# Kernel optimization log

Measured on AMD Instinct MI355X. Metric: run time of the kernel, lower is better.

Reference implementation:

```python
import jax, jax.numpy as jnp
import numpy as np

N_NODES, T, C_IN, B = 207, 12, 4, 4
NT = N_NODES * T
D, H = 96, 4
HD = D // H
FF = 4 * D
ENC_L, DEC_L = 4, 1
N_MASK = int(NT * 0.75)
N_UNMASK = NT - N_MASK
MAX_NEIGH = 40
ATTN_SCALE = 1.0 / float(np.sqrt(HD))
SQRT_D = float(np.sqrt(D))


def _ln(x, g, b, eps=1e-5):
    m = jnp.mean(x, -1, keepdims=True)
    v = jnp.mean((x - m) ** 2, -1, keepdims=True)
    return (x - m) * jax.lax.rsqrt(v + eps) * g + b


def _transformer(x, attn_mask, layers):
    # x: [B, S, D]; attn_mask: [S, S] bool (True = disallowed) or None.
    x = x * SQRT_D  # nn.Transformer-style input scaling
    def step(h, p):
        aw, ab, W1, B1, W2, B2, LN = p
        Bq, S, _ = h.shape
        q = (h @ aw[0] + ab[0]).reshape(Bq, S, H, HD)
        k = (h @ aw[1] + ab[1]).reshape(Bq, S, H, HD)
        v = (h @ aw[2] + ab[2]).reshape(Bq, S, H, HD)
        scores = jnp.einsum('bqhd,bkhd->bhqk', q, k) * ATTN_SCALE
        if attn_mask is not None:
            scores = jnp.where(attn_mask, jnp.float32(-1e30), scores)
        probs = jax.nn.softmax(scores, axis=-1)
        o = jnp.einsum('bhqk,bkhd->bqhd', probs, v).reshape(Bq, S, D)
        h = _ln(h + o @ aw[3] + ab[3], LN[0, 0], LN[0, 1])  # post-norm (torch default)
        f = jax.nn.relu(h @ W1 + B1) @ W2 + B2
        h = _ln(h + f, LN[1, 0], LN[1, 1])
        return h, None
    x, _ = jax.lax.scan(step, x, layers)
    return x


def _layer_params(key, nlayers):
    ks = jax.random.split(key, 3)
    attn_w = jax.random.normal(ks[0], (nlayers, 4, D, D), jnp.float32) / float(np.sqrt(D))
    w1 = jax.random.normal(ks[1], (nlayers, D, FF), jnp.float32) / float(np.sqrt(D))
    w2 = jax.random.normal(ks[2], (nlayers, FF, D), jnp.float32) / float(np.sqrt(FF))
    ln = jnp.broadcast_to(jnp.stack([jnp.ones(D), jnp.zeros(D)]), (nlayers, 2, 2, D)).astype(jnp.float32)
    return (attn_w, jnp.zeros((nlayers, 4, D), jnp.float32), w1,
            jnp.zeros((nlayers, FF), jnp.float32), w2, jnp.zeros((nlayers, D), jnp.float32), ln)


def setup_inputs() -> dict:
    key = jax.random.key(0)
    ks = jax.random.split(key, 12)
    rng = np.random.default_rng(42)
    perm = rng.permutation(NT)
    masked_idx = jnp.asarray(np.sort(perm[:N_MASK]), jnp.int32)
    unmasked_idx = jnp.asarray(np.sort(perm[N_MASK:]), jnp.int32)
    ea = _layer_params(ks[3], ENC_L)
    da = _layer_params(ks[4], DEC_L)
    return dict(
        history_data=jax.random.uniform(ks[0], (B, T, N_NODES, C_IN), jnp.float32),
        unmasked_idx=unmasked_idx, masked_idx=masked_idx,
        nodevec1=jax.random.normal(ks[1], (N_NODES, 10), jnp.float32),
        nodevec2=jax.random.normal(ks[2], (10, N_NODES), jnp.float32),
        dim_w=jax.random.normal(ks[5], (1, D), jnp.float32),
        dim_b=jnp.zeros((D,), jnp.float32),
        pos_emb=jax.random.uniform(ks[6], (NT, D), jnp.float32, -0.02, 0.02),
        tod_w=jax.random.normal(ks[7], (1, D), jnp.float32) * 0.02,
        tod_b=jnp.zeros((D,), jnp.float32),
        dow_w=jax.random.normal(ks[8], (1, D), jnp.float32) * 0.02,
        dow_b=jnp.zeros((D,), jnp.float32),
        mask_token=jax.random.normal(ks[9], (D,), jnp.float32) * 0.02,
        enc_attn_w=ea[0], enc_attn_b=ea[1], enc_ffn_w1=ea[2], enc_ffn_b1=ea[3],
        enc_ffn_w2=ea[4], enc_ffn_b2=ea[5], enc_ln=ea[6],
        enc_norm_g=jnp.ones((D,), jnp.float32), enc_norm_b=jnp.zeros((D,), jnp.float32),
        e2d_w=jax.random.normal(ks[10], (D, D), jnp.float32) / float(np.sqrt(D)),
        e2d_b=jnp.zeros((D,), jnp.float32),
        dec_attn_w=da[0], dec_attn_b=da[1], dec_ffn_w1=da[2], dec_ffn_b1=da[3],
        dec_ffn_w2=da[4], dec_ffn_b2=da[5], dec_ln=da[6],
        dec_norm_g=jnp.ones((D,), jnp.float32), dec_norm_b=jnp.zeros((D,), jnp.float32),
        out_w=jax.random.normal(ks[11], (D, 1), jnp.float32) / float(np.sqrt(D)),
        out_b=jnp.zeros((1,), jnp.float32),
    )


def reference(history_data, unmasked_idx, masked_idx, nodevec1, nodevec2,
              dim_w, dim_b, pos_emb, tod_w, tod_b, dow_w, dow_b, mask_token,
              enc_attn_w, enc_attn_b, enc_ffn_w1, enc_ffn_b1, enc_ffn_w2, enc_ffn_b2, enc_ln,
              enc_norm_g, enc_norm_b, e2d_w, e2d_b,
              dec_attn_w, dec_attn_b, dec_ffn_w1, dec_ffn_b1, dec_ffn_w2, dec_ffn_b2, dec_ln,
              dec_norm_g, dec_norm_b, out_w, out_b):
    hist = jnp.transpose(history_data, (0, 2, 3, 1))  # [B, N, C, T]
    tod = hist[:, :, 3:4, :].reshape(B, NT, 1)
    dow = hist[:, :, 2:3, :].reshape(B, NT, 1)
    # --- adaptive graph: softmax(relu(v1 v2)), threshold + top-40, straight-through ---
    A = jax.nn.softmax(jax.nn.relu(nodevec1 @ nodevec2), axis=1)
    kth = -jnp.sort(-A, axis=1)[:, MAX_NEIGH:MAX_NEIGH + 1]  # (MAX_NEIGH+1)-th largest per row
    keep = jnp.logical_and(A > 1.0 / N_NODES, A > kth).astype(A.dtype)
    bin_mask = jax.lax.stop_gradient(keep - A) + A
    adpA = A * bin_mask
    adpA_full = jnp.repeat(jnp.repeat(adpA, T, axis=0), T, axis=1)  # [NT, NT] block structure
    # --- embed + positional/temporal encoding ---
    x = jnp.transpose(hist[:, :, 0:1, :], (0, 1, 3, 2)) @ dim_w + dim_b  # [B, N, T, D]
    token = x.reshape(B, NT, D) + pos_emb + (tod @ tod_w + tod_b) + (dow @ dow_w + dow_b)
    # --- encoder over unmasked tokens with graph-derived attention mask ---
    enc_in = token[:, unmasked_idx, :]
    A_sub = adpA_full[unmasked_idx][:, unmasked_idx]
    attn_mask = A_sub == 0  # ~A.bool(): True = disallowed
    h = _transformer(enc_in, attn_mask,
                     (enc_attn_w, enc_attn_b, enc_ffn_w1, enc_ffn_b1, enc_ffn_w2, enc_ffn_b2, enc_ln))
    h = _ln(h, enc_norm_g, enc_norm_b)
    # --- decoder ---
    h = h @ e2d_w + e2d_b
    h_masked = (mask_token[None, None, :] + pos_emb[masked_idx]
                + (tod[:, masked_idx] @ tod_w + tod_b)
                + (dow[:, masked_idx] @ dow_w + dow_b))  # [B, N_MASK, D]
    full = jnp.concatenate([h, h_masked], axis=1)  # [B, NT, D]
    full = _transformer(full, None,
                        (dec_attn_w, dec_attn_b, dec_ffn_w1, dec_ffn_b1, dec_ffn_w2, dec_ffn_b2, dec_ln))
    full = _ln(full, dec_norm_g, dec_norm_b)
    recon = full @ out_w + out_b  # [B, NT, 1]
    recon_masked = recon[:, N_UNMASK:, :]
    label = jnp.transpose(hist, (0, 1, 3, 2))[:, :, :, 0].reshape(B, NT, 1)
    label_masked = label[:, masked_idx, :]
    return recon_masked, label_masked
```

## Files before the change

### kernel.cpp

```cpp
#include <hip/hip_runtime.h>
#include <math.h>

#define N_NODES 207
#define T_STEPS 12
#define NT 2484
#define BQ 4
#define DIM 96
#define NH 4
#define HD 24
#define FFD 384
#define N_MASK 1863
#define N_UNMASK 621
#define MAX_NEIGH 40
#define ATTN_SCALE 0.20412414523193154f
#define SQRT_DF 9.797958971132712f
#define KT 256
#define NMW 20
#define NBH 16

static inline int cdiv(int a, int b) { return (a + b - 1) / b; }

__global__ __launch_bounds__(256) void adj_kernel(const float* __restrict__ nv1,
                                                  const float* __restrict__ nv2,
                                                  float* __restrict__ keep) {
    int r = blockIdx.x, t = threadIdx.x;
    __shared__ float a[N_NODES];
    __shared__ float red[256];
    __shared__ int   redi[256];
    __shared__ int   taken[N_NODES];
    __shared__ float v1[10];
    __shared__ float kth;
    if (t < 10) v1[t] = nv1[r * 10 + t];
    __syncthreads();
    if (t < N_NODES) {
        float s = 0.f;
#pragma unroll
        for (int c = 0; c < 10; ++c) s += v1[c] * nv2[c * N_NODES + t];
        a[t] = fmaxf(s, 0.f);
        taken[t] = 0;
    }
    __syncthreads();
    red[t] = (t < N_NODES) ? a[t] : -3e38f;
    __syncthreads();
    for (int s = 128; s > 0; s >>= 1) {
        if (t < s) red[t] = fmaxf(red[t], red[t + s]);
        __syncthreads();
    }
    float mx = red[0];
    __syncthreads();
    float e = 0.f;
    if (t < N_NODES) e = __expf(a[t] - mx);
    red[t] = e;
    __syncthreads();
    for (int s = 128; s > 0; s >>= 1) {
        if (t < s) red[t] += red[t + s];
        __syncthreads();
    }
    float inv = 1.f / red[0];
    __syncthreads();
    if (t < N_NODES) a[t] = e * inv;
    __syncthreads();
    for (int round = 0; round <= MAX_NEIGH; ++round) {
        red[t]  = (t < N_NODES && !taken[t]) ? a[t] : -1.f;
        redi[t] = t;
        __syncthreads();
        for (int s = 128; s > 0; s >>= 1) {
            if (t < s && red[t + s] > red[t]) { red[t] = red[t + s]; redi[t] = redi[t + s]; }
            __syncthreads();
        }
        if (t == 0) {
            taken[redi[0]] = 1;
            if (round == MAX_NEIGH) kth = red[0];
        }
        __syncthreads();
    }
    if (t < N_NODES) {
        float av = a[t];
        keep[r * N_NODES + t] = (av > (1.f / 207.f) && av > kth) ? 1.f : 0.f;
    }
}

__global__ void maskbits_kernel(const float* __restrict__ keep, const int* __restrict__ uidx,
                                unsigned int* __restrict__ mw) {
    int q = blockIdx.x;
    int w = threadIdx.x;
    if (w >= NMW) return;
    const float* krow = keep + (uidx[q] / T_STEPS) * N_NODES;
    unsigned int word = 0;
    for (int j = 0; j < 32; ++j) {
        int k = w * 32 + j;
        if (k < N_UNMASK && krow[uidx[k] / T_STEPS] != 0.f) word |= (1u << j);
    }
    mw[q * NMW + w] = word;
}

__global__ void encin_kernel(const float* __restrict__ hist, const int* __restrict__ uidx,
                             const float* __restrict__ dim_w, const float* __restrict__ dim_b,
                             const float* __restrict__ pos,
                             const float* __restrict__ tod_w, const float* __restrict__ tod_b,
                             const float* __restrict__ dow_w, const float* __restrict__ dow_b,
                             float* __restrict__ h) {
    int idx = blockIdx.x * blockDim.x + threadIdx.x;
    if (idx >= BQ * N_UNMASK * DIM) return;
    int d = idx % DIM;
    int q = (idx / DIM) % N_UNMASK;
    int b = idx / (DIM * N_UNMASK);
    int u = uidx[q];
    int n = u / T_STEPS, t = u % T_STEPS;
    const float* hp = hist + ((size_t)(b * T_STEPS + t) * N_NODES + n) * 4;
    float h0 = hp[0], dw = hp[2], td = hp[3];
    float val = h0 * dim_w[d] + dim_b[d] + pos[u * DIM + d]
              + td * tod_w[d] + tod_b[d] + dw * dow_w[d] + dow_b[d];
    h[idx] = val * SQRT_DF;
}

__global__ void hmasked_kernel(const float* __restrict__ hist, const int* __restrict__ midx,
                               const float* __restrict__ mask_token, const float* __restrict__ pos,
                               const float* __restrict__ tod_w, const float* __restrict__ tod_b,
                               const float* __restrict__ dow_w, const float* __restrict__ dow_b,
                               float* __restrict__ full) {
    int idx = blockIdx.x * blockDim.x + threadIdx.x;
    if (idx >= BQ * N_MASK * DIM) return;
    int d = idx % DIM;
    int j = (idx / DIM) % N_MASK;
    int b = idx / (DIM * N_MASK);
    int m = midx[j];
    int n = m / T_STEPS, t = m % T_STEPS;
    const float* hp = hist + ((size_t)(b * T_STEPS + t) * N_NODES + n) * 4;
    float dw = hp[2], td = hp[3];
    float val = mask_token[d] + pos[m * DIM + d]
              + td * tod_w[d] + tod_b[d] + dw * dow_w[d] + dow_b[d];
    full[((size_t)(b * NT) + N_UNMASK + j) * DIM + d] = val * SQRT_DF;
}

__global__ void label_kernel(const float* __restrict__ hist, const int* __restrict__ midx,
                             float* __restrict__ out) {
    int idx = blockIdx.x * blockDim.x + threadIdx.x;
    if (idx >= BQ * N_MASK) return;
    int j = idx % N_MASK;
    int b = idx / N_MASK;
    int m = midx[j];
    int n = m / T_STEPS, t = m % T_STEPS;
    out[BQ * N_MASK + idx] = hist[((size_t)(b * T_STEPS + t) * N_NODES + n) * 4 + 0];
}

#define ACCROW(accv, av)                                          \
    accv.x += av.x*w0.x + av.y*w1.x + av.z*w2.x + av.w*w3.x;      \
    accv.y += av.x*w0.y + av.y*w1.y + av.z*w2.y + av.w*w3.y;      \
    accv.z += av.x*w0.z + av.y*w1.z + av.z*w2.z + av.w*w3.z;      \
    accv.w += av.x*w0.w + av.y*w1.w + av.z*w2.w + av.w*w3.w;

template<int WMODE, int LNA>
__global__ __launch_bounds__(256) void tgemm_kernel(const float* __restrict__ A,
                                                    const float* __restrict__ W,
                                                    const float* __restrict__ bias,
                                                    const float* __restrict__ res,
                                                    float* __restrict__ C,
                                                    int M, int N, int K, int gm,
                                                    int relu, float scale, int rmode,
                                                    const float* __restrict__ g1,
                                                    const float* __restrict__ b1,
                                                    const float* __restrict__ g2,
                                                    const float* __restrict__ b2,
                                                    float* __restrict__ wb) {
    __shared__ float As[64][100];
    __shared__ float Ws[96][64];
    __shared__ float lred[64][4];
    __shared__ float lmv[64][2];
    int tid = threadIdx.x;
    int bm = blockIdx.x % gm;
    int bn = blockIdx.x / gm;
    int m0 = bm * 64, n0 = bn * 64;
    int tn4 = (tid & 15) * 4;
    int tm4 = (tid >> 4) * 4;
    float4 acc0 = {0,0,0,0}, acc1 = {0,0,0,0}, acc2 = {0,0,0,0}, acc3 = {0,0,0,0};

    for (int kc = 0; kc < K; kc += 96) {
        if (kc) __syncthreads();
#pragma unroll
        for (int i = 0; i < 6; ++i) {
            int f = i * 256 + tid;
            int r = f / 24, c4 = (f % 24) * 4;
            float4 v = {0,0,0,0};
            if (m0 + r < M) v = *(const float4*)(A + (size_t)(m0 + r) * K + kc + c4);
            *(float4*)&As[r][c4] = v;
        }
#pragma unroll
        for (int i = 0; i < 6; ++i) {
            int f = i * 256 + tid;
            int kr = f >> 4, n4 = (f & 15) * 4;
            int gn = n0 + n4;
            float4 v = {0,0,0,0};
            if (gn < N) {
                if (WMODE == 0) {
                    v = *(const float4*)(W + (size_t)(kc + kr) * N + gn);
                } else {
                    int gg = gn / 96, nc = gn - gg * 96;
                    v = *(const float4*)(W + (size_t)gg * 9216 + (kc + kr) * 96 + nc);
                }
            }
            *(float4*)&Ws[kr][n4] = v;
        }
        __syncthreads();

        if (LNA > 0 && kc == 0) {
#pragma unroll
            for (int pass = 0; pass < LNA; ++pass) {
                const float* lg = pass ? g2 : g1;
                const float* lb = pass ? b2 : b1;
                int row = tid >> 2, part = tid & 3;
                float s = 0.f;
                for (int c = part * 24; c < part * 24 + 24; ++c) s += As[row][c];
                lred[row][part] = s;
                __syncthreads();
                float mean = (lred[row][0] + lred[row][1] + lred[row][2] + lred[row][3]) * (1.f / 96.f);
                float s2 = 0.f;
                for (int c = part * 24; c < part * 24 + 24; ++c) {
                    float d = As[row][c] - mean; s2 += d * d;
                }
                __syncthreads();
                lred[row][part] = s2;
                __syncthreads();
                if (part == 0) {
                    float var = (lred[row][0] + lred[row][1] + lred[row][2] + lred[row][3]) * (1.f / 96.f);
                    lmv[row][0] = mean;
                    lmv[row][1] = rsqrtf(var + 1e-5f);
                }
                __syncthreads();
#pragma unroll
                for (int i = 0; i < 6; ++i) {
                    int f = i * 256 + tid;
                    int r = f / 24, c4 = (f % 24) * 4;
                    float mn = lmv[r][0], rsd = lmv[r][1];
                    float4 v = *(float4*)&As[r][c4];
                    v.x = (v.x - mn) * rsd * lg[c4 + 0] + lb[c4 + 0];
                    v.y = (v.y - mn) * rsd * lg[c4 + 1] + lb[c4 + 1];
                    v.z = (v.z - mn) * rsd * lg[c4 + 2] + lb[c4 + 2];
                    v.w = (v.w - mn) * rsd * lg[c4 + 3] + lb[c4 + 3];
                    *(float4*)&As[r][c4] = v;
                }
                __syncthreads();
            }
            if (wb && bn == 0) {
#pragma unroll
                for (int i = 0; i < 6; ++i) {
                    int f = i * 256 + tid;
                    int r = f / 24, c4 = (f % 24) * 4;
                    if (m0 + r < M)
                        *(float4*)(wb + (size_t)(m0 + r) * 96 + c4) = *(const float4*)&As[r][c4];
                }
            }
        }

#pragma unroll 4
        for (int k = 0; k < 96; k += 4) {
            float4 a0 = *(const float4*)&As[tm4 + 0][k];
            float4 a1 = *(const float4*)&As[tm4 + 1][k];
            float4 a2 = *(const float4*)&As[tm4 + 2][k];
            float4 a3 = *(const float4*)&As[tm4 + 3][k];
            float4 w0 = *(const float4*)&Ws[k + 0][tn4];
            float4 w1 = *(const float4*)&Ws[k + 1][tn4];
            float4 w2 = *(const float4*)&Ws[k + 2][tn4];
            float4 w3 = *(const float4*)&Ws[k + 3][tn4];
            ACCROW(acc0, a0)
            ACCROW(acc1, a1)
            ACCROW(acc2, a2)
            ACCROW(acc3, a3)
        }
    }

    int gn = n0 + tn4;
    if (gn >= N) return;
    float4 bv = *(const float4*)(bias + gn);
    float4 av[4] = {acc0, acc1, acc2, acc3};
#pragma unroll
    for (int i = 0; i < 4; ++i) {
        int grow = m0 + tm4 + i;
        if (grow >= M) break;
        float4 acc = av[i];
        acc.x += bv.x; acc.y += bv.y; acc.z += bv.z; acc.w += bv.w;
        if (res) {
            int rr = grow;
            if (rmode) { int bb = grow / N_MASK; rr = bb * NT + N_UNMASK + (grow - bb * N_MASK); }
            float4 rv = *(const float4*)(res + (size_t)rr * N + gn);
            acc.x += rv.x; acc.y += rv.y; acc.z += rv.z; acc.w += rv.w;
        }
        if (relu) {
            acc.x = fmaxf(acc.x, 0.f); acc.y = fmaxf(acc.y, 0.f);
            acc.z = fmaxf(acc.z, 0.f); acc.w = fmaxf(acc.w, 0.f);
        }
        acc.x *= scale; acc.y *= scale; acc.z *= scale; acc.w *= scale;
        *(float4*)(C + (size_t)grow * N + gn) = acc;
    }
}

template<int QPL>
__global__ __launch_bounds__(256) void fattn_kernel(const float* __restrict__ Qp,
                                                    const float* __restrict__ Kp,
                                                    const float* __restrict__ Vp,
                                                    float* __restrict__ Pm,
                                                    float* __restrict__ Pl,
                                                    float* __restrict__ Pacc,
                                                    const unsigned int* __restrict__ maskw,
                                                    int swz,
                                                    int S, int Sq, int qoff,
                                                    int nqt, int NS, int rs) {
    __shared__ float smem[12288];
    float* Ks = smem;
    float* Vs = smem + 6144;

    int t = threadIdx.x;
    int w = t >> 6, lane = t & 63;
    int bid = blockIdx.x;
    int ns, qt, hh, b;
    if (swz) {
        int xcd = bid & 7, slot = bid >> 3;
        int spb = nqt * NS;
        int bh = xcd + 8 * (slot / spb);
        int r = slot % spb;
        qt = r / NS; ns = r % NS;
        b = bh >> 2; hh = bh & 3;
    } else {
        ns = bid % NS; int r1 = bid / NS;
        qt = r1 % nqt; r1 /= nqt;
        hh = r1 % NH; b = r1 / NH;
    }

    float qr[QPL][HD];
    bool qvalid[QPL];
#pragma unroll
    for (int h = 0; h < QPL; ++h) {
        int qidx = qt * (64 * QPL) + h * 64 + lane;
        qvalid[h] = qidx < Sq;
        if (qvalid[h]) {
            const float* qp = Qp + ((size_t)(b * S + qoff + qidx)) * rs + hh * HD;
#pragma unroll
            for (int i = 0; i < 6; ++i) {
                float4 v = *(const float4*)(qp + i * 4);
                qr[h][i*4+0] = v.x; qr[h][i*4+1] = v.y;
                qr[h][i*4+2] = v.z; qr[h][i*4+3] = v.w;
            }
        } else {
#pragma unroll
            for (int d = 0; d < HD; ++d) qr[h][d] = 0.f;
        }
    }

    float m[QPL], l[QPL];
    float acc[QPL][HD];
#pragma unroll
    for (int h = 0; h < QPL; ++h) {
        m[h] = -1e30f; l[h] = 0.f;
#pragma unroll
        for (int d = 0; d < HD; ++d) acc[h][d] = 0.f;
    }

    int ntile = (S + KT - 1) / KT;
    int tpn = (ntile + NS - 1) / NS;
    int c0 = ns * tpn;
    int c1 = min(c0 + tpn, ntile);

    for (int c = c0; c < c1; ++c) {
        __syncthreads();
        int base_k = c * KT;
#pragma unroll
        for (int i = 0; i < 6; ++i) {
            int fi = i * 256 + t;
            int row = fi / 6, cc = fi - row * 6;
            int gk = base_k + row;
            float4 kv = {0,0,0,0};
            float4 vv = {0,0,0,0};
            if (gk < S) {
                size_t roff = ((size_t)(b * S + gk)) * rs + hh * HD + cc * 4;
                kv = *(const float4*)(Kp + roff);
                vv = *(const float4*)(Vp + roff);
            }
            *(float4*)(Ks + row * HD + cc * 4) = kv;
            *(float4*)(Vs + row * HD + cc * 4) = vv;
        }
        __syncthreads();

        unsigned int mw0 = ~0u, mw1 = ~0u;
        if (QPL == 1 && maskw) {
            int qidx = qt * 64 + lane;
            if (qidx < Sq) {
                int wi = c * 8 + w * 2;
                mw0 = (wi     < NMW) ? maskw[qidx * NMW + wi]     : 0u;
                mw1 = (wi + 1 < NMW) ? maskw[qidx * NMW + wi + 1] : 0u;
            }
        }

        for (int g = 0; g < 16; ++g) {
            float sgrp[QPL][4];
            float pv[QPL][4];
#pragma unroll
            for (int j = 0; j < 4; ++j) {
                int j2 = g * 4 + j;
                int kk = (w << 6) + j2;
                int gk = base_k + kk;
                const float4* kr = (const float4*)(Ks + kk * HD);
                float d0[QPL];
#pragma unroll
                for (int h = 0; h < QPL; ++h) d0[h] = 0.f;
#pragma unroll
                for (int i = 0; i < 6; ++i) {
                    float4 kv = kr[i];
#pragma unroll
                    for (int h = 0; h < QPL; ++h) {
                        d0[h] += qr[h][i*4+0]*kv.x + qr[h][i*4+1]*kv.y
                               + qr[h][i*4+2]*kv.z + qr[h][i*4+3]*kv.w;
                    }
                }
#pragma unroll
                for (int h = 0; h < QPL; ++h) {
                    float s = d0[h] * ATTN_SCALE;
                    if (QPL == 1 && maskw) {
                        unsigned int wsel = (j2 & 32) ? mw1 : mw0;
                        if (!((wsel >> (j2 & 31)) & 1u)) s = -1e30f;
                    }
                    if (gk >= S) s = -INFINITY;
                    sgrp[h][j] = s;
                }
            }
#pragma unroll
            for (int h = 0; h < QPL; ++h) {
                float gmx = fmaxf(fmaxf(sgrp[h][0], sgrp[h][1]),
                                  fmaxf(sgrp[h][2], sgrp[h][3]));
                if (gmx > m[h]) {
                    float f = __expf(m[h] - gmx);
                    l[h] *= f;
#pragma unroll
                    for (int d = 0; d < HD; ++d) acc[h][d] *= f;
                    m[h] = gmx;
                }
#pragma unroll
                for (int j = 0; j < 4; ++j) {
                    float p = __expf(sgrp[h][j] - m[h]);
                    pv[h][j] = p;
                    l[h] += p;
                }
            }
#pragma unroll
            for (int j = 0; j < 4; ++j) {
                int kk = (w << 6) + g * 4 + j;
                const float4* vr = (const float4*)(Vs + kk * HD);
#pragma unroll
                for (int i = 0; i < 6; ++i) {
                    float4 vv = vr[i];
#pragma unroll
                    for (int h = 0; h < QPL; ++h) {
                        acc[h][i*4+0] += pv[h][j]*vv.x;
                        acc[h][i*4+1] += pv[h][j]*vv.y;
                        acc[h][i*4+2] += pv[h][j]*vv.z;
                        acc[h][i*4+3] += pv[h][j]*vv.w;
                    }
                }
            }
        }
    }

#pragma unroll
    for (int h = 0; h < QPL; ++h) {
        __syncthreads();
        float* my = smem + (size_t)(w * 64 + lane) * 27;
        my[0] = m[h]; my[1] = l[h];
#pragma unroll
        for (int d = 0; d < HD; ++d) my[2 + d] = acc[h][d];
        __syncthreads();
        if (t < 64) {
            int qidx = qt * (64 * QPL) + h * 64 + t;
            if (qidx < Sq) {
                float M2 = -INFINITY;
#pragma unroll
                for (int w2 = 0; w2 < 4; ++w2)
                    M2 = fmaxf(M2, smem[(size_t)(w2 * 64 + t) * 27]);
                float L = 0.f;
                float o[HD];
#pragma unroll
                for (int d = 0; d < HD; ++d) o[d] = 0.f;
#pragma unroll
                for (int w2 = 0; w2 < 4; ++w2) {
                    const float* pp = smem + (size_t)(w2 * 64 + t) * 27;
                    float f = __expf(pp[0] - M2);
                    L += pp[1] * f;
#pragma unroll
                    for (int d = 0; d < HD; ++d) o[d] += pp[2 + d] * f;
                }
                size_t pb = ((size_t)((b * NH + hh) * NS + ns)) * Sq + qidx;
                Pm[pb] = M2;
                Pl[pb] = L;
                float* pa = Pacc + pb * 24;
#pragma unroll
                for (int i = 0; i < 6; ++i)
                    *(float4*)(pa + i * 4) = make_float4(o[i*4+0], o[i*4+1],
                                                         o[i*4+2], o[i*4+3]);
            }
        }
    }
}

__global__ __launch_bounds__(256) void attn_combine_kernel(const float* __restrict__ Pm,
                                                           const float* __restrict__ Pl,
                                                           const float* __restrict__ Pacc,
                                                           float* __restrict__ O,
                                                           int Sq, int NS) {
    int tid = blockIdx.x * 256 + threadIdx.x;
    if (tid >= NBH * Sq * 6) return;
    int d4 = tid % 6;
    int q  = (tid / 6) % Sq;
    int bh = tid / (6 * Sq);
    float M = -1e30f;
    for (int ns = 0; ns < NS; ++ns)
        M = fmaxf(M, Pm[((size_t)bh * NS + ns) * Sq + q]);
    float L = 0.f;
    float ax = 0.f, ay = 0.f, az = 0.f, aw = 0.f;
    for (int ns = 0; ns < NS; ++ns) {
        size_t pb = ((size_t)bh * NS + ns) * Sq + q;
        float wgt = __expf(Pm[pb] - M);
        L += wgt * Pl[pb];
        float4 f0 = *(const float4*)(Pacc + pb * 24 + d4 * 4);
        ax += wgt * f0.x; ay += wgt * f0.y;
        az += wgt * f0.z; aw += wgt * f0.w;
    }
    float inv = 1.f / L;
    int b = bh >> 2, hh = bh & 3;
    float* op = O + ((size_t)(b * Sq + q)) * DIM + hh * HD + d4 * 4;
    *(float4*)op = make_float4(ax * inv, ay * inv, az * inv, aw * inv);
}

__global__ __launch_bounds__(256) void ln_kernel(const float* __restrict__ X,
                                                 const float* __restrict__ g,
                                                 const float* __restrict__ bta,
                                                 float* __restrict__ Y, int M) {
    int row = blockIdx.x * 4 + (threadIdx.x >> 6);
    if (row >= M) return;
    int lane = threadIdx.x & 63;
    const float* x = X + (size_t)row * DIM;
    float x0 = x[lane];
    float x1 = (lane < 32) ? x[64 + lane] : 0.f;
    float s = x0 + x1;
#pragma unroll
    for (int o = 32; o; o >>= 1) s += __shfl_xor(s, o);
    float mean = s * (1.f / DIM);
    float d0 = x0 - mean;
    float d1 = (lane < 32) ? (x1 - mean) : 0.f;
    float v = d0 * d0 + d1 * d1;
#pragma unroll
    for (int o = 32; o; o >>= 1) v += __shfl_xor(v, o);
    float rs = rsqrtf(v * (1.f / DIM) + 1e-5f);
    float* y = Y + (size_t)row * DIM;
    y[lane] = d0 * rs * g[lane] + bta[lane];
    if (lane < 32) y[64 + lane] = d1 * rs * g[64 + lane] + bta[64 + lane];
}

__global__ __launch_bounds__(256) void tail_kernel(const float* __restrict__ X,
                                                   const float* __restrict__ g1,
                                                   const float* __restrict__ b1,
                                                   const float* __restrict__ g2,
                                                   const float* __restrict__ b2,
                                                   const float* __restrict__ ow,
                                                   const float* __restrict__ ob,
                                                   float* __restrict__ out, int Mtail) {
    int row = blockIdx.x * 4 + (threadIdx.x >> 6);
    if (row >= Mtail) return;
    int lane = threadIdx.x & 63;
    bool lo = lane < 32;
    const float* x = X + (size_t)row * DIM;
    float x0 = x[lane];
    float x1 = lo ? x[64 + lane] : 0.f;
    float s = x0 + x1;
#pragma unroll
    for (int o = 32; o; o >>= 1) s += __shfl_xor(s, o);
    float mean = s * (1.f / DIM);
    float d0 = x0 - mean;
    float d1 = lo ? (x1 - mean) : 0.f;
    float v = d0 * d0 + d1 * d1;
#pragma unroll
    for (int o = 32; o; o >>= 1) v += __shfl_xor(v, o);
    float rs = rsqrtf(v * (1.f / DIM) + 1e-5f);
    float y0 = d0 * rs * g1[lane] + b1[lane];
    float y1 = lo ? (d1 * rs * g1[64 + lane] + b1[64 + lane]) : 0.f;
    s = y0 + y1;
#pragma unroll
    for (int o = 32; o; o >>= 1) s += __shfl_xor(s, o);
    mean = s * (1.f / DIM);
    d0 = y0 - mean;
    d1 = lo ? (y1 - mean) : 0.f;
    v = d0 * d0 + d1 * d1;
#pragma unroll
    for (int o = 32; o; o >>= 1) v += __shfl_xor(v, o);
    rs = rsqrtf(v * (1.f / DIM) + 1e-5f);
    float z0 = d0 * rs * g2[lane] + b2[lane];
    float z1 = lo ? (d1 * rs * g2[64 + lane] + b2[64 + lane]) : 0.f;
    float a = z0 * ow[lane] + (lo ? z1 * ow[64 + lane] : 0.f);
#pragma unroll
    for (int o = 32; o; o >>= 1) a += __shfl_xor(a, o);
    if (lane == 0) out[row] = a + ob[0];
}

__global__ void copy_enc_kernel(const float* __restrict__ src, float* __restrict__ full) {
    int idx = blockIdx.x * blockDim.x + threadIdx.x;
    if (idx >= BQ * N_UNMASK * DIM) return;
    int d = idx % DIM;
    int q = (idx / DIM) % N_UNMASK;
    int b = idx / (DIM * N_UNMASK);
    full[((size_t)(b * NT) + q) * DIM + d] = src[idx];
}

extern "C" void kernel_launch(void* const* d_in, const int* in_sizes, int n_in,
                              void* d_out, int out_size, void* d_ws, size_t ws_size,
                              hipStream_t stream) {
    const float* hist   = (const float*)d_in[0];
    const int*   uidx   = (const int*)d_in[1];
    const int*   midx   = (const int*)d_in[2];
    const float* nv1    = (const float*)d_in[3];
    const float* nv2    = (const float*)d_in[4];
    const float* dim_w  = (const float*)d_in[5];
    const float* dim_b  = (const float*)d_in[6];
    const float* pos    = (const float*)d_in[7];
    const float* tod_w  = (const float*)d_in[8];
    const float* tod_b  = (const float*)d_in[9];
    const float* dow_w  = (const float*)d_in[10];
    const float* dow_b  = (const float*)d_in[11];
    const float* mtok   = (const float*)d_in[12];
    const float* eaw    = (const float*)d_in[13];
    const float* eab    = (const float*)d_in[14];
    const float* ew1    = (const float*)d_in[15];
    const float* eb1    = (const float*)d_in[16];
    const float* ew2    = (const float*)d_in[17];
    const float* eb2    = (const float*)d_in[18];
    const float* eln    = (const float*)d_in[19];
    const float* eng    = (const float*)d_in[20];
    const float* enb    = (const float*)d_in[21];
    const float* e2dw   = (const float*)d_in[22];
    const float* e2db   = (const float*)d_in[23];
    const float* daw    = (const float*)d_in[24];
    const float* dab    = (const float*)d_in[25];
    const float* dw1    = (const float*)d_in[26];
    const float* db1    = (const float*)d_in[27];
    const float* dw2    = (const float*)d_in[28];
    const float* db2    = (const float*)d_in[29];
    const float* dln    = (const float*)d_in[30];
    const float* dng    = (const float*)d_in[31];
    const float* dnb    = (const float*)d_in[32];
    const float* ow     = (const float*)d_in[33];
    const float* ob     = (const float*)d_in[34];

    float* ws = (float*)d_ws;
    float*        keep  = ws;
    unsigned int* maskw = (unsigned int*)(ws + 44032);
    float* eh = ws + 56576;
    float* e1 = ws + 295040;
    float* e2 = ws + 1248896;
    float* et = ws + 1487360;
    float* fh = ws + 1725824;
    float* qf = ws + 2679680;
    float* dh = ws + 5541248;
    float* dt = ws + 6256640;
    float* PaccE = ws + 5541248;
    float* PmE   = ws + 6256640;
    float* PlE   = ws + 6286448;
    float* PaccD = ws + 56576;
    float* PmD   = ws + 1487360;
    float* PlD   = ws + 1546976;
    float* dLN   = e1;

    float* outp = (float*)d_out;
    const int ME = BQ * N_UNMASK;
    const int MD = BQ * NT;
    const int MT = BQ * N_MASK;
    const int gmE = cdiv(ME, 64);
    const int gmD = cdiv(MD, 64);
    const int gmT = cdiv(MT, 64);
    const int NSE = 3, NSD = 2;
    const int nqtE = 10;
    const int nqtD = 15;

    adj_kernel<<<N_NODES, 256, 0, stream>>>(nv1, nv2, keep);
    maskbits_kernel<<<N_UNMASK, 32, 0, stream>>>(keep, uidx, maskw);
    encin_kernel<<<cdiv(ME * DIM, 256), 256, 0, stream>>>(
        hist, uidx, dim_w, dim_b, pos, tod_w, tod_b, dow_w, dow_b, eh);
    label_kernel<<<cdiv(MT, 256), 256, 0, stream>>>(hist, midx, outp);

    for (int l = 0; l < 4; ++l) {
        const float* aw = eaw + (size_t)l * 4 * DIM * DIM;
        const float* ab = eab + (size_t)l * 4 * DIM;
        if (l == 0) {
            tgemm_kernel<1,0><<<gmE * 5, 256, 0, stream>>>(
                eh, aw, ab, nullptr, e1, ME, 288, 96, gmE, 0, 1.f, 0,
                nullptr, nullptr, nullptr, nullptr, nullptr);
        } else {
            tgemm_kernel<1,1><<<gmE * 5, 256, 0, stream>>>(
                et, aw, ab, nullptr, e1, ME, 288, 96, gmE, 0, 1.f, 0,
                eln + (size_t)((l - 1) * 4 + 2) * DIM,
                eln + (size_t)((l - 1) * 4 + 3) * DIM,
                nullptr, nullptr, eh);
        }
        fattn_kernel<1><<<NBH * nqtE * NSE, 256, 0, stream>>>(
            e1, e1 + 96, e1 + 192, PmE, PlE, PaccE, maskw, 1,
            N_UNMASK, N_UNMASK, 0, nqtE, NSE, 288);
        attn_combine_kernel<<<cdiv(NBH * N_UNMASK * 6, 256), 256, 0, stream>>>(
            PmE, PlE, PaccE, e2, N_UNMASK, NSE);
        tgemm_kernel<0,0><<<gmE * 2, 256, 0, stream>>>(
            e2, aw + 3 * DIM * DIM, ab + 3 * DIM, eh, et, ME, 96, 96, gmE, 0, 1.f, 0,
            nullptr, nullptr, nullptr, nullptr, nullptr);
        ln_kernel<<<cdiv(ME, 4), 256, 0, stream>>>(
            et, eln + (size_t)(l * 4 + 0) * DIM, eln + (size_t)(l * 4 + 1) * DIM, eh, ME);
        tgemm_kernel<0,0><<<gmE * 6, 256, 0, stream>>>(
            eh, ew1 + (size_t)l * DIM * FFD, eb1 + (size_t)l * FFD, nullptr, e1,
            ME, FFD, 96, gmE, 1, 1.f, 0,
            nullptr, nullptr, nullptr, nullptr, nullptr);
        tgemm_kernel<0,0><<<gmE * 2, 256, 0, stream>>>(
            e1, ew2 + (size_t)l * FFD * DIM, eb2 + (size_t)l * DIM, eh, et,
            ME, 96, FFD, gmE, 0, 1.f, 0,
            nullptr, nullptr, nullptr, nullptr, nullptr);
    }
    tgemm_kernel<0,2><<<gmE * 2, 256, 0, stream>>>(
        et, e2dw, e2db, nullptr, e2, ME, 96, 96, gmE, 0, SQRT_DF, 0,
        eln + (size_t)(3 * 4 + 2) * DIM, eln + (size_t)(3 * 4 + 3) * DIM,
        eng, enb, nullptr);
    copy_enc_kernel<<<cdiv(ME * DIM, 256), 256, 0, stream>>>(e2, fh);
    hmasked_kernel<<<cdiv(MT * DIM, 256), 256, 0, stream>>>(
        hist, midx, mtok, pos, tod_w, tod_b, dow_w, dow_b, fh);

    tgemm_kernel<1,0><<<gmD * 5, 256, 0, stream>>>(
        fh, daw, dab, nullptr, qf, MD, 288, 96, gmD, 0, 1.f, 0,
        nullptr, nullptr, nullptr, nullptr, nullptr);
    fattn_kernel<2><<<NBH * nqtD * NSD, 256, 0, stream>>>(
        qf, qf + 96, qf + 192, PmD, PlD, PaccD, nullptr, 1,
        NT, N_MASK, N_UNMASK, nqtD, NSD, 288);
    attn_combine_kernel<<<cdiv(NBH * N_MASK * 6, 256), 256, 0, stream>>>(
        PmD, PlD, PaccD, dh, N_MASK, NSD);
    tgemm_kernel<0,0><<<gmT * 2, 256, 0, stream>>>(
        dh, daw + 3 * DIM * DIM, dab + 3 * DIM, fh, dt, MT, 96, 96, gmT, 0, 1.f, 1,
        nullptr, nullptr, nullptr, nullptr, nullptr);
    ln_kernel<<<cdiv(MT, 4), 256, 0, stream>>>(dt, dln + 0 * DIM, dln + 1 * DIM, dLN, MT);
    tgemm_kernel<0,0><<<gmT * 6, 256, 0, stream>>>(
        dLN, dw1, db1, nullptr, qf, MT, FFD, 96, gmT, 1, 1.f, 0,
        nullptr, nullptr, nullptr, nullptr, nullptr);
    tgemm_kernel<0,0><<<gmT * 2, 256, 0, stream>>>(
        qf, dw2, db2, dLN, dh, MT, 96, FFD, gmT, 0, 1.f, 0,
        nullptr, nullptr, nullptr, nullptr, nullptr);
    tail_kernel<<<cdiv(MT, 4), 256, 0, stream>>>(
        dh, dln + 2 * DIM, dln + 3 * DIM, dng, dnb, ow, ob, outp, MT);
}
```

Baseline: 688.2 us.

## Fuse post-attention LayerNorm into FFN GEMM and raise decoder attention split

After: 740.1 us. 7.5% more time.

```diff
diff --git a/kernel.cpp b/kernel.cpp
--- a/kernel.cpp
+++ b/kernel.cpp
@@ -300,7 +300,9 @@
                                                     const float* __restrict__ Vp,
                                                     float* __restrict__ Pm,
                                                     float* __restrict__ Pl,
-                                                    float* __restrict__ Pacc,
+                                                    float* __restrict__ PaccA,
+                                                    float* __restrict__ PaccB,
+                                                    int nsSplit,
                                                     const unsigned int* __restrict__ maskw,
                                                     int swz,
                                                     int S, int Sq, int qoff,
@@ -356,11 +358,7 @@
     }
 
     int ntile = (S + KT - 1) / KT;
-    int tpn = (ntile + NS - 1) / NS;
-    int c0 = ns * tpn;
-    int c1 = min(c0 + tpn, ntile);
-
-    for (int c = c0; c < c1; ++c) {
+    for (int c = ns; c < ntile; c += NS) {
         __syncthreads();
         int base_k = c * KT;
 #pragma unroll
@@ -486,10 +484,13 @@
 #pragma unroll
                     for (int d = 0; d < HD; ++d) o[d] += pp[2 + d] * f;
                 }
-                size_t pb = ((size_t)((b * NH + hh) * NS + ns)) * Sq + qidx;
-                Pm[pb] = M2;
-                Pl[pb] = L;
-                float* pa = Pacc + pb * 24;
+                int bh = b * NH + hh;
+                size_t pq = ((size_t)(ns * NBH + bh)) * Sq + qidx;
+                Pm[pq] = M2;
+                Pl[pq] = L;
+                float* pa = (ns < nsSplit)
+                    ? PaccA + pq * 24
+                    : PaccB + (((size_t)((ns - nsSplit) * NBH + bh)) * Sq + qidx) * 24;
 #pragma unroll
                 for (int i = 0; i < 6; ++i)
                     *(float4*)(pa + i * 4) = make_float4(o[i*4+0], o[i*4+1],
@@ -501,7 +502,9 @@
 
 __global__ __launch_bounds__(256) void attn_combine_kernel(const float* __restrict__ Pm,
                                                            const float* __restrict__ Pl,
-                                                           const float* __restrict__ Pacc,
+                                                           const float* __restrict__ PaccA,
+                                                           const float* __restrict__ PaccB,
+                                                           int nsSplit,
                                                            float* __restrict__ O,
                                                            int Sq, int NS) {
     int tid = blockIdx.x * 256 + threadIdx.x;
@@ -511,14 +514,17 @@
     int bh = tid / (6 * Sq);
     float M = -1e30f;
     for (int ns = 0; ns < NS; ++ns)
-        M = fmaxf(M, Pm[((size_t)bh * NS + ns) * Sq + q]);
+        M = fmaxf(M, Pm[((size_t)(ns * NBH + bh)) * Sq + q]);
     float L = 0.f;
     float ax = 0.f, ay = 0.f, az = 0.f, aw = 0.f;
     for (int ns = 0; ns < NS; ++ns) {
-        size_t pb = ((size_t)bh * NS + ns) * Sq + q;
-        float wgt = __expf(Pm[pb] - M);
-        L += wgt * Pl[pb];
-        float4 f0 = *(const float4*)(Pacc + pb * 24 + d4 * 4);
+        size_t pq = ((size_t)(ns * NBH + bh)) * Sq + q;
+        float wgt = __expf(Pm[pq] - M);
+        L += wgt * Pl[pq];
+        const float* pa = (ns < nsSplit)
+            ? PaccA + pq * 24
+            : PaccB + (((size_t)((ns - nsSplit) * NBH + bh)) * Sq + q) * 24;
+        float4 f0 = *(const float4*)(pa + d4 * 4);
         ax += wgt * f0.x; ay += wgt * f0.y;
         az += wgt * f0.z; aw += wgt * f0.w;
     }
@@ -526,31 +532,6 @@
     int b = bh >> 2, hh = bh & 3;
     float* op = O + ((size_t)(b * Sq + q)) * DIM + hh * HD + d4 * 4;
     *(float4*)op = make_float4(ax * inv, ay * inv, az * inv, aw * inv);
-}
-
-__global__ __launch_bounds__(256) void ln_kernel(const float* __restrict__ X,
-                                                 const float* __restrict__ g,
-                                                 const float* __restrict__ bta,
-                                                 float* __restrict__ Y, int M) {
-    int row = blockIdx.x * 4 + (threadIdx.x >> 6);
-    if (row >= M) return;
-    int lane = threadIdx.x & 63;
-    const float* x = X + (size_t)row * DIM;
-    float x0 = x[lane];
-    float x1 = (lane < 32) ? x[64 + lane] : 0.f;
-    float s = x0 + x1;
-#pragma unroll
-    for (int o = 32; o; o >>= 1) s += __shfl_xor(s, o);
-    float mean = s * (1.f / DIM);
-    float d0 = x0 - mean;
-    float d1 = (lane < 32) ? (x1 - mean) : 0.f;
-    float v = d0 * d0 + d1 * d1;
-#pragma unroll
-    for (int o = 32; o; o >>= 1) v += __shfl_xor(v, o);
-    float rs = rsqrtf(v * (1.f / DIM) + 1e-5f);
-    float* y = Y + (size_t)row * DIM;
-    y[lane] = d0 * rs * g[lane] + bta[lane];
-    if (lane < 32) y[64 + lane] = d1 * rs * g[64 + lane] + bta[64 + lane];
 }
 
 __global__ __launch_bounds__(256) void tail_kernel(const float* __restrict__ X,
@@ -660,10 +641,12 @@
     float* PaccE = ws + 5541248;
     float* PmE   = ws + 6256640;
     float* PlE   = ws + 6286448;
-    float* PaccD = ws + 56576;
-    float* PmD   = ws + 1487360;
-    float* PlD   = ws + 1546976;
-    float* dLN   = e1;
+    float* PaccDA = ws + 56576;
+    float* PmD    = ws + 1487360;
+    float* PlD    = ws + 1576784;
+    float* PaccDB = ws + 5541248;
+    float* dY = ws + 56576;
+    float* dZ = ws + 771968;
 
     float* outp = (float*)d_out;
     const int ME = BQ * N_UNMASK;
@@ -672,7 +655,7 @@
     const int gmE = cdiv(ME, 64);
     const int gmD = cdiv(MD, 64);
     const int gmT = cdiv(MT, 64);
-    const int NSE = 3, NSD = 2;
+    const int NSE = 3, NSD = 3;
     const int nqtE = 10;
     const int nqtD = 15;
 
@@ -697,19 +680,18 @@
                 nullptr, nullptr, eh);
         }
         fattn_kernel<1><<<NBH * nqtE * NSE, 256, 0, stream>>>(
-            e1, e1 + 96, e1 + 192, PmE, PlE, PaccE, maskw, 1,
+            e1, e1 + 96, e1 + 192, PmE, PlE, PaccE, nullptr, NSE, maskw, 1,
             N_UNMASK, N_UNMASK, 0, nqtE, NSE, 288);
         attn_combine_kernel<<<cdiv(NBH * N_UNMASK * 6, 256), 256, 0, stream>>>(
-            PmE, PlE, PaccE, e2, N_UNMASK, NSE);
+            PmE, PlE, PaccE, nullptr, NSE, e2, N_UNMASK, NSE);
         tgemm_kernel<0,0><<<gmE * 2, 256, 0, stream>>>(
             e2, aw + 3 * DIM * DIM, ab + 3 * DIM, eh, et, ME, 96, 96, gmE, 0, 1.f, 0,
             nullptr, nullptr, nullptr, nullptr, nullptr);
-        ln_kernel<<<cdiv(ME, 4), 256, 0, stream>>>(
-            et, eln + (size_t)(l * 4 + 0) * DIM, eln + (size_t)(l * 4 + 1) * DIM, eh, ME);
-        tgemm_kernel<0,0><<<gmE * 6, 256, 0, stream>>>(
-            eh, ew1 + (size_t)l * DIM * FFD, eb1 + (size_t)l * FFD, nullptr, e1,
+        tgemm_kernel<0,1><<<gmE * 6, 256, 0, stream>>>(
+            et, ew1 + (size_t)l * DIM * FFD, eb1 + (size_t)l * FFD, nullptr, e1,
             ME, FFD, 96, gmE, 1, 1.f, 0,
-            nullptr, nullptr, nullptr, nullptr, nullptr);
+            eln + (size_t)(l * 4 + 0) * DIM, eln + (size_t)(l * 4 + 1) * DIM,
+            nullptr, nullptr, eh);
         tgemm_kernel<0,0><<<gmE * 2, 256, 0, stream>>>(
             e1, ew2 + (size_t)l * FFD * DIM, eb2 + (size_t)l * DIM, eh, et,
             ME, 96, FFD, gmE, 0, 1.f, 0,
@@ -727,19 +709,18 @@
         fh, daw, dab, nullptr, qf, MD, 288, 96, gmD, 0, 1.f, 0,
         nullptr, nullptr, nullptr, nullptr, nullptr);
     fattn_kernel<2><<<NBH * nqtD * NSD, 256, 0, stream>>>(
-        qf, qf + 96, qf + 192, PmD, PlD, PaccD, nullptr, 1,
+        qf, qf + 96, qf + 192, PmD, PlD, PaccDA, PaccDB, 2, nullptr, 1,
         NT, N_MASK, N_UNMASK, nqtD, NSD, 288);
     attn_combine_kernel<<<cdiv(NBH * N_MASK * 6, 256), 256, 0, stream>>>(
-        PmD, PlD, PaccD, dh, N_MASK, NSD);
+        PmD, PlD, PaccDA, PaccDB, 2, dt, N_MASK, NSD);
     tgemm_kernel<0,0><<<gmT * 2, 256, 0, stream>>>(
-        dh, daw + 3 * DIM * DIM, dab + 3 * DIM, fh, dt, MT, 96, 96, gmT, 0, 1.f, 1,
+        dt, daw + 3 * DIM * DIM, dab + 3 * DIM, fh, dY, MT, 96, 96, gmT, 0, 1.f, 1,
         nullptr, nullptr, nullptr, nullptr, nullptr);
-    ln_kernel<<<cdiv(MT, 4), 256, 0, stream>>>(dt, dln + 0 * DIM, dln + 1 * DIM, dLN, MT);
-    tgemm_kernel<0,0><<<gmT * 6, 256, 0, stream>>>(
-        dLN, dw1, db1, nullptr, qf, MT, FFD, 96, gmT, 1, 1.f, 0,
-        nullptr, nullptr, nullptr, nullptr, nullptr);
+    tgemm_kernel<0,1><<<gmT * 6, 256, 0, stream>>>(
+        dY, dw1, db1, nullptr, qf, MT, FFD, 96, gmT, 1, 1.f, 0,
+        dln + 0 * DIM, dln + 1 * DIM, nullptr, nullptr, dZ);
     tgemm_kernel<0,0><<<gmT * 2, 256, 0, stream>>>(
-        qf, dw2, db2, dLN, dh, MT, 96, FFD, gmT, 0, 1.f, 0,
+        qf, dw2, db2, dZ, dh, MT, 96, FFD, gmT, 0, 1.f, 0,
         nullptr, nullptr, nullptr, nullptr, nullptr);
     tail_kernel<<<cdiv(MT, 4), 256, 0, stream>>>(
         dh, dln + 2 * DIM, dln + 3 * DIM, dng, dnb, ow, ob, outp, MT);
```
